# Performance work log

Hardware: AMD Instinct MI355X
Metric: run time of the kernel (lower is better)

Reference implementation:

```python
import jax, jax.numpy as jnp
import numpy as np

EPS = 1e-5

def setup_inputs() -> dict:
    key = jax.random.key(0)
    k1, k2, k3, k4, k5 = jax.random.split(key, 5)
    B, S, D, N = 4, 512, 768, 64
    return {
        "x": jax.random.uniform(k1, (B, S, D), dtype=jnp.float32),
        "A": jax.random.uniform(k2, (D, N), dtype=jnp.float32),
        "B_weight_raw": jax.random.normal(k3, (N, D), dtype=jnp.float32),
        "C_weight_raw": jax.random.normal(k4, (D, N), dtype=jnp.float32),
        "norm_gamma_raw": jax.random.normal(k5, (D,), dtype=jnp.float32),
    }

def reference(x, A, B_weight_raw, C_weight_raw, norm_gamma_raw):
    # x: [B, S, D]
    Bsz, S, D = x.shape
    N = A.shape[1]
    A_gate = jax.nn.sigmoid(A)                      # [D, N]
    Bw = jax.nn.sigmoid(B_weight_raw)               # [N, D] (TopologicalLinear: sigmoid-constrained weights)
    Cw = jax.nn.sigmoid(C_weight_raw)               # [D, N]
    gamma = jax.nn.sigmoid(norm_gamma_raw)          # [D]  (TopologicalNorm: layernorm w/ sigmoid scale)

    h0 = jnp.zeros((Bsz, D, N), dtype=x.dtype)

    def step(h, x_t):
        # x_t: [B, D]
        inp = x_t @ Bw.T                            # [B, N]
        morph = inp[:, None, :] * x_t[:, :, None]   # [B, D, N]
        h = jnp.clip(h * A_gate + morph, 0.0, 1.0)  # bounded state update
        y = jnp.sum(h * Cw, axis=-1)                # [B, D]
        mu = jnp.mean(y, axis=-1, keepdims=True)
        var = jnp.var(y, axis=-1, keepdims=True)
        y = (y - mu) * jax.lax.rsqrt(var + EPS) * gamma
        return h, y

    h_final, ys = jax.lax.scan(step, h0, jnp.swapaxes(x, 0, 1))  # ys: [S, B, D]
    y = jnp.swapaxes(ys, 0, 1)                                    # [B, S, D]
    return jnp.clip(y + x, 0.0, 1.0), h_final
```

## Files before the change

kernel.cpp:

```cpp
#include <hip/hip_runtime.h>
#include <math.h>

#define DD 768
#define NN 64
#define SS 512
#define BB 4
#define BSD (BB * SS * DD)

__device__ __forceinline__ float sigmf(float v) { return 1.0f / (1.0f + expf(-v)); }

template <int CTRL>
__device__ __forceinline__ float dppadd(float v) {
    int s = __builtin_amdgcn_update_dpp(0, __float_as_int(v), CTRL, 0xF, 0xF, true);
    return v + __int_as_float(s);
}
__device__ __forceinline__ float row_sum15(float v) {
    v = dppadd<0x111>(v);
    v = dppadd<0x112>(v);
    v = dppadd<0x114>(v);
    v = dppadd<0x118>(v);
    return v;
}
__device__ __forceinline__ float wave_sum63(float v) {
    v = row_sum15(v);
    v = dppadd<0x142>(v);
    v = dppadd<0x143>(v);
    return v;
}

__global__ __launch_bounds__(256) void prep_kernel(const float* __restrict__ Braw,
                                                   const float* __restrict__ graw,
                                                   float* __restrict__ BwT,
                                                   float* __restrict__ gamma_s) {
    __shared__ float tile[64][65];
    int tx = threadIdx.x & 63;
    int tq = threadIdx.x >> 6;
    int d0 = blockIdx.x * 64;
#pragma unroll
    for (int i = 0; i < 16; ++i) {
        int n = tq + i * 4;
        tile[n][tx] = sigmf(Braw[n * DD + d0 + tx]);
    }
    __syncthreads();
#pragma unroll
    for (int i = 0; i < 16; ++i) {
        int dl = tq + i * 4;
        BwT[(d0 + dl) * NN + tx] = tile[tx][dl];
    }
    int gi = blockIdx.x * 256 + threadIdx.x;
    if (gi < DD) gamma_s[gi] = sigmf(graw[gi]);
}

__global__ __launch_bounds__(256, 2) void inp_xpose_kernel(const float* __restrict__ x,
                                                           const float* __restrict__ BwT,
                                                           float* __restrict__ inp,
                                                           float* __restrict__ xT) {
    __shared__ float4 smem[2048];

    if (blockIdx.x < 512) {
        float4* bwlds0 = smem;
        float4* bwlds1 = smem + 1024;
        int w    = threadIdx.x >> 6;
        int lane = threadIdx.x & 63;
        int g = lane >> 4;
        int q = lane & 15;
        int r = blockIdx.x * 4 + w;
        const float*  xr  = x + (size_t)r * DD;
        const float4* bwg = (const float4*)BwT;

#pragma unroll
        for (int k = 0; k < 4; ++k)
            bwlds0[threadIdx.x + k * 256] = bwg[threadIdx.x + k * 256];
        __syncthreads();

        float4 acc = {0.f, 0.f, 0.f, 0.f};
        for (int c = 0; c < 12; ++c) {
            float4* cur = (c & 1) ? bwlds1 : bwlds0;
            float4* nxt = (c & 1) ? bwlds0 : bwlds1;
            float4 s0, s1, s2, s3;
            if (c < 11) {
                int base = (c + 1) * 1024 + threadIdx.x;
                s0 = bwg[base];
                s1 = bwg[base + 256];
                s2 = bwg[base + 512];
                s3 = bwg[base + 768];
            }
            int d0 = c * 64;
#pragma unroll
            for (int jj = 0; jj < 4; ++jj) {
                int dbase = jj * 16 + g;
                float x0 = xr[d0 + dbase + 0];
                float x1 = xr[d0 + dbase + 4];
                float x2 = xr[d0 + dbase + 8];
                float x3 = xr[d0 + dbase + 12];
                float4 w0 = cur[(dbase + 0) * 16 + q];
                float4 w1 = cur[(dbase + 4) * 16 + q];
                float4 w2 = cur[(dbase + 8) * 16 + q];
                float4 w3 = cur[(dbase + 12) * 16 + q];
#define IFMA(W, X)                       \
    acc.x = fmaf(X, W.x, acc.x);         \
    acc.y = fmaf(X, W.y, acc.y);         \
    acc.z = fmaf(X, W.z, acc.z);         \
    acc.w = fmaf(X, W.w, acc.w);
                IFMA(w0, x0) IFMA(w1, x1) IFMA(w2, x2) IFMA(w3, x3)
            }
            if (c < 11) {
                nxt[threadIdx.x]       = s0;
                nxt[threadIdx.x + 256] = s1;
                nxt[threadIdx.x + 512] = s2;
                nxt[threadIdx.x + 768] = s3;
            }
            __syncthreads();
        }

#pragma unroll
        for (int off = 16; off <= 32; off <<= 1) {
            acc.x += __shfl_xor(acc.x, off, 64);
            acc.y += __shfl_xor(acc.y, off, 64);
            acc.z += __shfl_xor(acc.z, off, 64);
            acc.w += __shfl_xor(acc.w, off, 64);
        }
        if (lane < 16) ((float4*)(inp + (size_t)r * NN))[q] = acc;
    } else {
        float* tile = (float*)smem;
        int bidx = blockIdx.x - 512;
        int b  = bidx / 96;
        int r  = bidx - b * 96;
        int t0 = (r / 12) * 64;
        int d0 = (r % 12) * 64;
        int tx = threadIdx.x & 63;
        int tq = threadIdx.x >> 6;
#pragma unroll
        for (int i = 0; i < 16; ++i) {
            int t = tq + i * 4;
            tile[t * 65 + tx] = x[((size_t)b * SS + t0 + t) * DD + d0 + tx];
        }
        __syncthreads();
#pragma unroll
        for (int i = 0; i < 16; ++i) {
            int dl = tq + i * 4;
            xT[((size_t)b * DD + d0 + dl) * SS + t0 + tx] = tile[tx * 65 + dl];
        }
    }
}

__global__ __launch_bounds__(256, 3) void scan_kernel(const float* __restrict__ xT,
                                                      const float* __restrict__ Araw,
                                                      const float* __restrict__ Craw,
                                                      const float* __restrict__ inp,
                                                      float* __restrict__ Y,
                                                      float* __restrict__ hfin) {
    int w    = threadIdx.x >> 6;
    int lane = threadIdx.x & 63;
    int gb = blockIdx.x;
    int b  = gb / 192;
    int dg = gb - b * 192;
    int d  = dg * 4 + w;

    float a = sigmf(Araw[(size_t)d * NN + lane]);
    float c = sigmf(Craw[(size_t)d * NN + lane]);

    const float*  ip_ptr = inp + (size_t)(b * SS) * NN + lane;
    const float4* xt4    = (const float4*)(xT + ((size_t)b * DD + d) * SS);
    float*        y_d    = Y + (size_t)(b * SS) * DD + d;

    __shared__ float lds[4][2][8][68];

    int s8 = lane >> 3;
    int j8 = lane & 7;

    float Ai[8], Bi[8], Ci[8], Di[8];
    float4 Ax0, Ax1, Bx0, Bx1, Cx0, Cx1, Dx0, Dx1;
    float h = 0.f;

#define SPREF(P, T0)                                                       \
    {                                                                      \
        int tt_ = ((T0) < SS) ? (T0) : 0;                                  \
        _Pragma("unroll")                                                  \
        for (int i_ = 0; i_ < 8; ++i_) P##i[i_] = ip_ptr[(tt_ + i_) * NN]; \
        P##x0 = xt4[(tt_ >> 2) + 0];                                       \
        P##x1 = xt4[(tt_ >> 2) + 1];                                       \
    }
#define SCHUNK(P, T0, SL)                                                         \
    {                                                                             \
        const float xs_[8] = {P##x0.x, P##x0.y, P##x0.z, P##x0.w,                 \
                              P##x1.x, P##x1.y, P##x1.z, P##x1.w};                \
        _Pragma("unroll")                                                         \
        for (int i_ = 0; i_ < 8; ++i_) {                                          \
            h = __builtin_amdgcn_fmed3f(fmaf(h, a, P##i[i_] * xs_[i_]), 0.f, 1.f); \
            lds[w][SL][i_][lane] = h * c;                                         \
        }                                                                         \
        float4 v0_ = *(const float4*)&lds[w][SL][s8][j8 * 8];                     \
        float4 v1_ = *(const float4*)&lds[w][SL][s8][j8 * 8 + 4];                 \
        float s_ = ((v0_.x + v0_.y) + (v0_.z + v0_.w)) +                          \
                   ((v1_.x + v1_.y) + (v1_.z + v1_.w));                           \
        s_ = dppadd<0x111>(s_);                                                   \
        s_ = dppadd<0x112>(s_);                                                   \
        s_ = dppadd<0x114>(s_);                                                   \
        if (j8 == 7) y_d[((T0) + s8) * DD] = s_;                                  \
    }

    SPREF(A, 0)
    SPREF(B, 8)
    SPREF(C, 16)
    SPREF(D, 24)

    for (int t0 = 0; t0 < SS; t0 += 32) {
        SCHUNK(A, t0, 0)      SPREF(A, t0 + 32)
        SCHUNK(B, t0 + 8, 1)  SPREF(B, t0 + 40)
        SCHUNK(C, t0 + 16, 0) SPREF(C, t0 + 48)
        SCHUNK(D, t0 + 24, 1) SPREF(D, t0 + 56)
    }
    hfin[((size_t)b * DD + d) * NN + lane] = h;
}

__global__ __launch_bounds__(256) void scan_fb_kernel(const float* __restrict__ x,
                                                      const float* __restrict__ Araw,
                                                      const float* __restrict__ Craw,
                                                      const float* __restrict__ inp,
                                                      float* __restrict__ Y,
                                                      float* __restrict__ hfin) {
    int wid  = (blockIdx.x * 256 + threadIdx.x) >> 6;
    int lane = threadIdx.x & 63;
    int b = wid / DD;
    int d = wid - b * DD;

    float a = sigmf(Araw[d * NN + lane]);
    float c = sigmf(Craw[d * NN + lane]);

    const float* ip_ptr = inp + (b * SS) * NN + lane;
    const float* x_ptr  = x   + (b * SS) * DD + d;
    float*       y_ptr  = Y   + (b * SS) * DD + d;

    float cip[8], cxv[8], nip[8], nxv[8];
#pragma unroll
    for (int i = 0; i < 8; ++i) {
        cip[i] = ip_ptr[i * NN];
        cxv[i] = x_ptr[i * DD];
    }
    float h = 0.f;
    for (int t0 = 0; t0 < SS; t0 += 8) {
        int tn = t0 + 8;
        if (tn >= SS) tn = SS - 8;
#pragma unroll
        for (int i = 0; i < 8; ++i) {
            nip[i] = ip_ptr[(tn + i) * NN];
            nxv[i] = x_ptr[(tn + i) * DD];
        }
#pragma unroll
        for (int i = 0; i < 8; ++i) {
            h = __builtin_amdgcn_fmed3f(fmaf(h, a, cip[i] * cxv[i]), 0.f, 1.f);
            float v = wave_sum63(h * c);
            if (lane == 63) y_ptr[(t0 + i) * DD] = v;
        }
#pragma unroll
        for (int i = 0; i < 8; ++i) { cip[i] = nip[i]; cxv[i] = nxv[i]; }
    }
    hfin[(size_t)wid * NN + lane] = h;
}

__global__ __launch_bounds__(256) void ln_kernel(const float* __restrict__ x,
                                                 const float* __restrict__ gamma_s,
                                                 float* __restrict__ out) {
    int wid  = (blockIdx.x * 256 + threadIdx.x) >> 6;
    int lane = threadIdx.x & 63;
    float*       yr = out + (size_t)wid * DD;
    const float* xr = x   + (size_t)wid * DD;

    float4 y0 = ((const float4*)yr)[lane * 3 + 0];
    float4 y1 = ((const float4*)yr)[lane * 3 + 1];
    float4 y2 = ((const float4*)yr)[lane * 3 + 2];

    float s = ((y0.x + y0.y) + (y0.z + y0.w)) + ((y1.x + y1.y) + (y1.z + y1.w)) +
              ((y2.x + y2.y) + (y2.z + y2.w));
#pragma unroll
    for (int off = 32; off; off >>= 1) s += __shfl_xor(s, off, 64);
    float mu = s * (1.f / 768.f);

    float q = 0.f;
#define QACC(v)                 \
    {                           \
        float d0_ = (v) - mu;   \
        q = fmaf(d0_, d0_, q);  \
    }
    QACC(y0.x) QACC(y0.y) QACC(y0.z) QACC(y0.w)
    QACC(y1.x) QACC(y1.y) QACC(y1.z) QACC(y1.w)
    QACC(y2.x) QACC(y2.y) QACC(y2.z) QACC(y2.w)
#pragma unroll
    for (int off = 32; off; off >>= 1) q += __shfl_xor(q, off, 64);
    float inv = rsqrtf(q * (1.f / 768.f) + 1e-5f);

    float4 g0 = ((const float4*)gamma_s)[lane * 3 + 0];
    float4 g1 = ((const float4*)gamma_s)[lane * 3 + 1];
    float4 g2 = ((const float4*)gamma_s)[lane * 3 + 2];
    float4 x0 = ((const float4*)xr)[lane * 3 + 0];
    float4 x1 = ((const float4*)xr)[lane * 3 + 1];
    float4 x2 = ((const float4*)xr)[lane * 3 + 2];

#define FIN(yv, gv, xv) __builtin_amdgcn_fmed3f(fmaf((yv - mu) * inv, gv, xv), 0.f, 1.f)
    float4 o0, o1, o2;
    o0.x = FIN(y0.x, g0.x, x0.x); o0.y = FIN(y0.y, g0.y, x0.y);
    o0.z = FIN(y0.z, g0.z, x0.z); o0.w = FIN(y0.w, g0.w, x0.w);
    o1.x = FIN(y1.x, g1.x, x1.x); o1.y = FIN(y1.y, g1.y, x1.y);
    o1.z = FIN(y1.z, g1.z, x1.z); o1.w = FIN(y1.w, g1.w, x1.w);
    o2.x = FIN(y2.x, g2.x, x2.x); o2.y = FIN(y2.y, g2.y, x2.y);
    o2.z = FIN(y2.z, g2.z, x2.z); o2.w = FIN(y2.w, g2.w, x2.w);

    ((float4*)yr)[lane * 3 + 0] = o0;
    ((float4*)yr)[lane * 3 + 1] = o1;
    ((float4*)yr)[lane * 3 + 2] = o2;
}

extern "C" void kernel_launch(void* const* d_in, const int* in_sizes, int n_in,
                              void* d_out, int out_size, void* d_ws, size_t ws_size,
                              hipStream_t stream) {
    const float* x    = (const float*)d_in[0];
    const float* Araw = (const float*)d_in[1];
    const float* Braw = (const float*)d_in[2];
    const float* Craw = (const float*)d_in[3];
    const float* graw = (const float*)d_in[4];

    float* out  = (float*)d_out;
    float* hfin = out + (size_t)BSD;

    float* ws      = (float*)d_ws;
    float* BwT     = ws;
    float* gamma_s = ws + DD * NN;
    float* inp     = ws + DD * NN + DD;
    float* xT      = ws + DD * NN + DD + BB * SS * NN;

    size_t need = (size_t)(DD * NN + DD + (size_t)BB * SS * NN + (size_t)BSD) * sizeof(float);

    if (ws_size >= need) {
        prep_kernel<<<DD / 64, 256, 0, stream>>>(Braw, graw, BwT, gamma_s);
        inp_xpose_kernel<<<512 + BB * (SS / 64) * (DD / 64), 256, 0, stream>>>(
            x, BwT, inp, xT);
        scan_kernel<<<BB * (DD / 4), 256, 0, stream>>>(xT, Araw, Craw, inp, out, hfin);
    } else {
        prep_kernel<<<DD / 64, 256, 0, stream>>>(Braw, graw, BwT, gamma_s);
        inp_xpose_kernel<<<512 + BB * (SS / 64) * (DD / 64), 256, 0, stream>>>(
            x, BwT, inp, xT);
        scan_fb_kernel<<<(BB * DD * NN) / 256, 256, 0, stream>>>(x, Araw, Craw, inp, out, hfin);
    }
    ln_kernel<<<(BB * SS * NN) / 256, 256, 0, stream>>>(x, gamma_s, out);
}
```

Baseline: 61.28 us.

## Split scan over time halves with redundant recompute and regroup lanes across waves

Each (batch, 4-channel group) block is duplicated into two blocks. The second block recomputes the first 256 timesteps of the state without producing output, then emits the outputs for the second half, so the grid doubles. Lanes are regrouped so that each wave covers 4 channels × 16 state entries, and the per-step reduction becomes DPP row sums followed by a cross-wave LDS combine behind __syncthreads. This adds redundant recurrence work and a block-wide barrier every 8 steps in exchange for more parallel blocks and fewer LDS writes per step.

```diff
diff --git a/kernel.cpp b/kernel.cpp
--- a/kernel.cpp
+++ b/kernel.cpp
@@ -144,33 +144,34 @@
     }
 }
 
-__global__ __launch_bounds__(256, 3) void scan_kernel(const float* __restrict__ xT,
-                                                      const float* __restrict__ Araw,
-                                                      const float* __restrict__ Craw,
-                                                      const float* __restrict__ inp,
-                                                      float* __restrict__ Y,
-                                                      float* __restrict__ hfin) {
-    int w    = threadIdx.x >> 6;
+__global__ __launch_bounds__(256) void scan_kernel(const float* __restrict__ xT,
+                                                   const float* __restrict__ Araw,
+                                                   const float* __restrict__ Craw,
+                                                   const float* __restrict__ inp,
+                                                   float* __restrict__ Y,
+                                                   float* __restrict__ hfin) {
+    int p    = threadIdx.x >> 6;
     int lane = threadIdx.x & 63;
-    int gb = blockIdx.x;
+    int dl = lane >> 4;
+    int ng = lane & 15;
+    int half = blockIdx.x & 1;
+    int gb   = blockIdx.x >> 1;
     int b  = gb / 192;
     int dg = gb - b * 192;
-    int d  = dg * 4 + w;
-
-    float a = sigmf(Araw[(size_t)d * NN + lane]);
-    float c = sigmf(Craw[(size_t)d * NN + lane]);
-
-    const float*  ip_ptr = inp + (size_t)(b * SS) * NN + lane;
+    int d  = dg * 4 + dl;
+    int n  = p * 16 + ng;
+
+    float a = sigmf(Araw[(size_t)d * NN + n]);
+    float c = sigmf(Craw[(size_t)d * NN + n]);
+
+    const float*  ip_ptr = inp + (size_t)(b * SS) * NN + n;
     const float4* xt4    = (const float4*)(xT + ((size_t)b * DD + d) * SS);
-    float*        y_d    = Y + (size_t)(b * SS) * DD + d;
-
-    __shared__ float lds[4][2][8][68];
-
-    int s8 = lane >> 3;
-    int j8 = lane & 7;
-
-    float Ai[8], Bi[8], Ci[8], Di[8];
-    float4 Ax0, Ax1, Bx0, Bx1, Cx0, Cx1, Dx0, Dx1;
+    float*        y_blk  = Y + (size_t)(b * SS) * DD + dg * 4;
+
+    __shared__ float lds[2][4][4][8];
+
+    float Ai[8], Bi[8];
+    float4 Ax0, Ax1, Bx0, Bx1;
     float h = 0.f;
 
 #define SPREF(P, T0)                                                       \
@@ -181,37 +182,62 @@
         P##x0 = xt4[(tt_ >> 2) + 0];                                       \
         P##x1 = xt4[(tt_ >> 2) + 1];                                       \
     }
-#define SCHUNK(P, T0, SL)                                                         \
-    {                                                                             \
-        const float xs_[8] = {P##x0.x, P##x0.y, P##x0.z, P##x0.w,                 \
-                              P##x1.x, P##x1.y, P##x1.z, P##x1.w};                \
-        _Pragma("unroll")                                                         \
-        for (int i_ = 0; i_ < 8; ++i_) {                                          \
+#define HCH(P)                                                                   \
+    {                                                                            \
+        const float xs_[8] = {P##x0.x, P##x0.y, P##x0.z, P##x0.w,                \
+                              P##x1.x, P##x1.y, P##x1.z, P##x1.w};               \
+        _Pragma("unroll")                                                        \
+        for (int i_ = 0; i_ < 8; ++i_)                                           \
             h = __builtin_amdgcn_fmed3f(fmaf(h, a, P##i[i_] * xs_[i_]), 0.f, 1.f); \
-            lds[w][SL][i_][lane] = h * c;                                         \
-        }                                                                         \
-        float4 v0_ = *(const float4*)&lds[w][SL][s8][j8 * 8];                     \
-        float4 v1_ = *(const float4*)&lds[w][SL][s8][j8 * 8 + 4];                 \
-        float s_ = ((v0_.x + v0_.y) + (v0_.z + v0_.w)) +                          \
-                   ((v1_.x + v1_.y) + (v1_.z + v1_.w));                           \
-        s_ = dppadd<0x111>(s_);                                                   \
-        s_ = dppadd<0x112>(s_);                                                   \
-        s_ = dppadd<0x114>(s_);                                                   \
-        if (j8 == 7) y_d[((T0) + s8) * DD] = s_;                                  \
-    }
-
-    SPREF(A, 0)
-    SPREF(B, 8)
-    SPREF(C, 16)
-    SPREF(D, 24)
-
-    for (int t0 = 0; t0 < SS; t0 += 32) {
-        SCHUNK(A, t0, 0)      SPREF(A, t0 + 32)
-        SCHUNK(B, t0 + 8, 1)  SPREF(B, t0 + 40)
-        SCHUNK(C, t0 + 16, 0) SPREF(C, t0 + 48)
-        SCHUNK(D, t0 + 24, 1) SPREF(D, t0 + 56)
-    }
-    hfin[((size_t)b * DD + d) * NN + lane] = h;
+    }
+#define SCHUNK(P, T0, SL)                                                        \
+    {                                                                            \
+        const float xs_[8] = {P##x0.x, P##x0.y, P##x0.z, P##x0.w,                \
+                              P##x1.x, P##x1.y, P##x1.z, P##x1.w};               \
+        float hs_[8];                                                            \
+        _Pragma("unroll")                                                        \
+        for (int i_ = 0; i_ < 8; ++i_) {                                         \
+            h = __builtin_amdgcn_fmed3f(fmaf(h, a, P##i[i_] * xs_[i_]), 0.f, 1.f); \
+            hs_[i_] = h;                                                         \
+        }                                                                        \
+        float ps_[8];                                                            \
+        _Pragma("unroll")                                                        \
+        for (int i_ = 0; i_ < 8; ++i_) ps_[i_] = hs_[i_] * c;                    \
+        _Pragma("unroll")                                                        \
+        for (int i_ = 0; i_ < 8; ++i_) ps_[i_] = row_sum15(ps_[i_]);             \
+        if (ng == 15) {                                                          \
+            _Pragma("unroll")                                                    \
+            for (int i_ = 0; i_ < 8; ++i_) lds[SL][p][dl][i_] = ps_[i_];         \
+        }                                                                        \
+        __syncthreads();                                                         \
+        if (threadIdx.x < 32) {                                                  \
+            int i_  = threadIdx.x >> 2;                                          \
+            int dli = threadIdx.x & 3;                                           \
+            float v_ = (lds[SL][0][dli][i_] + lds[SL][1][dli][i_]) +             \
+                       (lds[SL][2][dli][i_] + lds[SL][3][dli][i_]);              \
+            y_blk[((T0) + i_) * DD + dli] = v_;                                  \
+        }                                                                        \
+    }
+
+    if (half) {
+        SPREF(A, 0)
+        SPREF(B, 8)
+        for (int t0 = 0; t0 < 256; t0 += 16) {
+            HCH(A) SPREF(A, t0 + 16)
+            HCH(B) SPREF(B, t0 + 24)
+        }
+    }
+
+    int tb = half * 256;
+    SPREF(A, tb)
+    SPREF(B, tb + 8)
+    for (int t0 = tb; t0 < tb + 256; t0 += 16) {
+        SCHUNK(A, t0, 0)
+        SPREF(A, t0 + 16)
+        SCHUNK(B, t0 + 8, 1)
+        SPREF(B, t0 + 24)
+    }
+    if (half) hfin[((size_t)b * DD + d) * NN + n] = h;
 }
 
 __global__ __launch_bounds__(256) void scan_fb_kernel(const float* __restrict__ x,
@@ -335,7 +361,7 @@
         prep_kernel<<<DD / 64, 256, 0, stream>>>(Braw, graw, BwT, gamma_s);
         inp_xpose_kernel<<<512 + BB * (SS / 64) * (DD / 64), 256, 0, stream>>>(
             x, BwT, inp, xT);
-        scan_kernel<<<BB * (DD / 4), 256, 0, stream>>>(xT, Araw, Craw, inp, out, hfin);
+        scan_kernel<<<BB * (DD / 4) * 2, 256, 0, stream>>>(xT, Araw, Craw, inp, out, hfin);
     } else {
         prep_kernel<<<DD / 64, 256, 0, stream>>>(Braw, graw, BwT, gamma_s);
         inp_xpose_kernel<<<512 + BB * (SS / 64) * (DD / 64), 256, 0, stream>>>(
```

Result: slower. 85.18 us (+39.0%).
